# Optimization experiments

Hardware: AMD Instinct MI355X
Metric: run time of the kernel (lower is better)

## Reference

```python
import jax, jax.numpy as jnp
import numpy as np

N_NODES = 100000


def gcn_conv(x, W, b, src, dst, num_nodes):
    # PyG GCNConv: add self-loops, symmetric deg^-1/2 normalization,
    # linear transform, scatter-add aggregation at dst, then bias.
    loop = jnp.arange(num_nodes, dtype=src.dtype)
    row = jnp.concatenate([src, loop])  # message sources
    col = jnp.concatenate([dst, loop])  # message destinations
    deg = jax.ops.segment_sum(jnp.ones_like(col, dtype=x.dtype), col,
                              num_segments=num_nodes)
    dinv = jnp.where(deg > 0, jax.lax.rsqrt(deg), 0.0)
    norm = dinv[row] * dinv[col]  # [E+N]
    h = x @ W  # [N, out]
    msg = h[row] * norm[:, None]  # gather + scale, [E+N, out]
    out = jax.ops.segment_sum(msg, col, num_segments=num_nodes)  # scatter-add
    return out + b


def setup_inputs() -> dict:
    key = jax.random.key(0)
    k1, k2, k3, k4, k5, k6 = jax.random.split(key, 6)
    dim_in, dim_h = 256, 128
    E = 1600000
    x = jax.random.normal(k1, (N_NODES, dim_in), dtype=jnp.float32)
    edge_index = jax.random.randint(k2, (2, E), 0, N_NODES, dtype=jnp.int64)
    # Glorot-style init for GCNConv weights
    W1 = jax.random.normal(k3, (dim_in, dim_h), dtype=jnp.float32) * (1.0 / np.sqrt(dim_in))
    b1 = jnp.zeros((dim_h,), dtype=jnp.float32)
    W2 = jax.random.normal(k4, (dim_h, 1), dtype=jnp.float32) * (1.0 / np.sqrt(dim_h))
    b2 = jnp.zeros((1,), dtype=jnp.float32)
    return {"x": x, "edge_index": edge_index, "W1": W1, "b1": b1, "W2": W2, "b2": b2}


def reference(x, edge_index, W1, b1, W2, b2):
    src, dst = edge_index[0], edge_index[1]
    h = gcn_conv(x, W1, b1, src, dst, N_NODES)
    h = jax.nn.relu(h)
    h = gcn_conv(h, W2, b2, src, dst, N_NODES)
    return jax.nn.sigmoid(h)  # [N, 1]
```

## Files before the change

kernel.cpp:

```cpp
#include <hip/hip_runtime.h>
#include <math.h>

#define NN 100000
#define DIN 256
#define DH 128
#define GEMM_NB 1563
#define BSHIFT 9
#define BNODES 512
#define NB_BUCKET 196
#define BCAP 12288
#define PA_EDGES 8192
#define PREP_NB 64

using short8  = __attribute__((ext_vector_type(8))) short;
using float4v = __attribute__((ext_vector_type(4))) float;

static __device__ __forceinline__ unsigned short f2bf(float f) {
    unsigned u = __float_as_uint(f);
    unsigned r = u + 0x7fffu + ((u >> 16) & 1u);
    return (unsigned short)(r >> 16);
}
static __device__ __forceinline__ float bf_lo(unsigned u) { return __uint_as_float(u << 16); }
static __device__ __forceinline__ float bf_hi(unsigned u) { return __uint_as_float(u & 0xffff0000u); }

__global__ __launch_bounds__(512) void k_prep_partA(const float* __restrict__ W1,
                                                    unsigned short* __restrict__ W1p,
                                                    const int* __restrict__ src,
                                                    const int* __restrict__ dst, int E,
                                                    int* __restrict__ bucketFill,
                                                    int2* __restrict__ bucketArr) {
    __shared__ int aCnt[NB_BUCKET];
    __shared__ int aBase[NB_BUCKET];
    const int tid = threadIdx.x;

    if (blockIdx.x < PREP_NB) {
        int t = blockIdx.x * 512 + tid;
        int lane = t & 63;
        int ks   = (t >> 6) & 7;
        int nt   = (t >> 9) & 1;
        int wv   = (t >> 10) & 3;
        int n = wv * 32 + nt * 16 + (lane & 15);
        int kbase = ks * 32 + (lane >> 4) * 8;
        short8 v;
#pragma unroll
        for (int j = 0; j < 8; ++j) v[j] = (short)f2bf(W1[(kbase + j) * DH + n]);
        *(short8*)&W1p[(long long)t * 8] = v;
        return;
    }

    const int ba = blockIdx.x - PREP_NB;
    for (int i = tid; i < NB_BUCKET; i += 512) aCnt[i] = 0;
    __syncthreads();
    const int e0   = ba * PA_EDGES;
    const int eend = min(e0 + PA_EDGES, E);
    for (int e = e0 + tid; e < eend; e += 512)
        atomicAdd(&aCnt[dst[e] >> BSHIFT], 1);
    __syncthreads();
    for (int i = tid; i < NB_BUCKET; i += 512) {
        int c = aCnt[i];
        aBase[i] = c ? atomicAdd(&bucketFill[i], c) : 0;
        aCnt[i] = 0;
    }
    __syncthreads();
    for (int e = e0 + tid; e < eend; e += 512) {
        int d = dst[e];
        int b = d >> BSHIFT;
        int r = atomicAdd(&aCnt[b], 1);
        bucketArr[(long long)b * BCAP + aBase[b] + r] = make_int2(src[e], d);
    }
}

__global__ __launch_bounds__(512) void k_gemm_partB(const float* __restrict__ x,
                                                    const unsigned short* __restrict__ W1p,
                                                    unsigned short* __restrict__ hs,
                                                    const int* __restrict__ bucketFill,
                                                    const int2* __restrict__ bucketArr,
                                                    int* __restrict__ cnt,
                                                    int* __restrict__ excl,
                                                    float* __restrict__ dinv,
                                                    int* __restrict__ eidx) {
    __shared__ unsigned short aL[64 * 32 * 8];
    __shared__ int h[BNODES];
    __shared__ int hex[BNODES];
    __shared__ int st[256];
    const int tid = threadIdx.x;

    if (blockIdx.x < NB_BUCKET) {
        const int b     = blockIdx.x;
        const int nbase = b << BSHIFT;
        const int len   = bucketFill[b];
        const long long abase = (long long)b * BCAP;

        if (tid < 256) st[tid] = (tid < b) ? bucketFill[tid] : 0;
        __syncthreads();
        for (int off = 128; off > 0; off >>= 1) {
            if (tid < off) st[tid] += st[tid + off];
            __syncthreads();
        }
        const int gbase = st[0];
        __syncthreads();

        for (int i = tid; i < BNODES; i += 512) h[i] = 0;
        __syncthreads();
        for (int k = tid; k < len; k += 512)
            atomicAdd(&h[bucketArr[abase + k].y - nbase], 1);
        __syncthreads();

        int a0 = 0, a1 = 0;
        if (tid < 256) {
            a0 = h[2 * tid]; a1 = h[2 * tid + 1];
            st[tid] = a0 + a1;
        }
        __syncthreads();
        for (int off = 1; off < 256; off <<= 1) {
            int val = (tid < 256 && tid >= off) ? st[tid - off] : 0;
            __syncthreads();
            if (tid < 256) st[tid] += val;
            __syncthreads();
        }
        if (tid < 256) {
            int prev = (tid > 0) ? st[tid - 1] : 0;
            hex[2 * tid]     = prev;
            hex[2 * tid + 1] = prev + a0;
        }
        __syncthreads();

        for (int i = tid; i < BNODES; i += 512) {
            int n = nbase + i;
            if (n < NN) {
                int c = h[i];
                cnt[n]  = c;
                excl[n] = gbase + hex[i];
                dinv[n] = rsqrtf(1.0f + (float)c);
            }
        }
        for (int i = tid; i < BNODES; i += 512) h[i] = 0;
        __syncthreads();

        for (int k = tid; k < len; k += 512) {
            int2 p = bucketArr[abase + k];
            int li = p.y - nbase;
            int r = atomicAdd(&h[li], 1);
            eidx[gbase + hex[li] + r] = p.x;
        }
        return;
    }

    const int bid  = blockIdx.x - NB_BUCKET;
    const int w8   = tid >> 6;
    const int lane = tid & 63;
    const int quad = lane >> 4;
    const int m16  = lane & 15;
    const int row0 = bid * 64;

    short8 bfr[8];
#pragma unroll
    for (int ks = 0; ks < 8; ++ks)
        bfr[ks] = ((const short8*)W1p)[(w8 * 8 + ks) * 64 + lane];

#pragma unroll
    for (int it = 0; it < 4; ++it) {
        int id  = it * 512 + tid;
        int row = id >> 5;
        int kb  = id & 31;
        int gr  = row0 + row;
        float4 f0, f1;
        if (gr < NN) {
            const float* xp = &x[(long long)gr * DIN + kb * 8];
            f0 = *(const float4*)xp;
            f1 = *(const float4*)(xp + 4);
        } else {
            f0 = make_float4(0.f, 0.f, 0.f, 0.f);
            f1 = f0;
        }
        short8 v;
        v[0] = (short)f2bf(f0.x); v[1] = (short)f2bf(f0.y);
        v[2] = (short)f2bf(f0.z); v[3] = (short)f2bf(f0.w);
        v[4] = (short)f2bf(f1.x); v[5] = (short)f2bf(f1.y);
        v[6] = (short)f2bf(f1.z); v[7] = (short)f2bf(f1.w);
        int chunk = row * 32 + (kb ^ (row & 31));
        *(short8*)&aL[chunk * 8] = v;
    }
    __syncthreads();

    float4v acc[4];
#pragma unroll
    for (int mt = 0; mt < 4; ++mt) acc[mt] = (float4v)(0.0f);

#pragma unroll
    for (int mt = 0; mt < 4; ++mt) {
        int row = mt * 16 + m16;
#pragma unroll
        for (int ks = 0; ks < 8; ++ks) {
            int kb = ks * 4 + quad;
            int chunk = row * 32 + (kb ^ (row & 31));
            short8 a = *(const short8*)&aL[chunk * 8];
            acc[mt] = __builtin_amdgcn_mfma_f32_16x16x32_bf16(a, bfr[ks], acc[mt], 0, 0, 0);
        }
    }

    const int n0 = w8 * 16;
#pragma unroll
    for (int mt = 0; mt < 4; ++mt) {
#pragma unroll
        for (int r = 0; r < 4; ++r) {
            int row = row0 + mt * 16 + quad * 4 + r;
            if (row < NN)
                hs[(long long)row * DH + n0 + m16] = f2bf(acc[mt][r]);
        }
    }
}

__global__ __launch_bounds__(256) void k_agg1l2(const int* __restrict__ eidx,
                                                const int* __restrict__ excl,
                                                const int* __restrict__ cnt,
                                                const unsigned* __restrict__ hs2,
                                                const float* __restrict__ dinv,
                                                const float* __restrict__ b1,
                                                const float* __restrict__ W2,
                                                float* __restrict__ zs) {
    int w = (blockIdx.x * 256 + threadIdx.x) >> 6;
    if (w >= NN) return;
    int lane = threadIdx.x & 63;
    int offs = __builtin_amdgcn_readfirstlane(excl[w]);
    int c    = __builtin_amdgcn_readfirstlane(cnt[w]);

    float dw = dinv[w];
    unsigned u = hs2[(long long)w * 64 + lane];
    float ax = dw * bf_lo(u);
    float ay = dw * bf_hi(u);

    const int l16 = lane & 15;
    for (int j = 0; j < c; j += 16) {
        int rem = c - j; if (rem > 16) rem = 16;
        int idx = offs + j + ((l16 < rem) ? l16 : 0);
        int sv = eidx[idx];
        float es[16]; unsigned uu[16];
#pragma unroll
        for (int q = 0; q < 16; ++q) if (q < rem) {
            int sq = __builtin_amdgcn_readlane(sv, q);
            es[q] = dinv[sq];
            uu[q] = hs2[(long long)sq * 64 + lane];
        }
#pragma unroll
        for (int q = 0; q < 16; ++q) if (q < rem) {
            ax = fmaf(es[q], bf_lo(uu[q]), ax);
            ay = fmaf(es[q], bf_hi(uu[q]), ay);
        }
    }

    float2 bb = ((const float2*)b1)[lane];
    float2 ww = ((const float2*)W2)[lane];
    float r0 = fmaxf(fmaf(dw, ax, bb.x), 0.0f);
    float r1 = fmaxf(fmaf(dw, ay, bb.y), 0.0f);
    float v = r0 * ww.x + r1 * ww.y;
#pragma unroll
    for (int off = 32; off > 0; off >>= 1) v += __shfl_down(v, off);
    if (lane == 0) zs[w] = v * dw;
}

__global__ void k_agg2_final(const int* __restrict__ eidx,
                             const int* __restrict__ excl,
                             const int* __restrict__ cnt,
                             const float* __restrict__ zs,
                             const float* __restrict__ dinv,
                             const float* __restrict__ b2,
                             float* __restrict__ out) {
    int i = blockIdx.x * 256 + threadIdx.x;
    if (i >= NN) return;
    int offs = excl[i];
    int c = cnt[i];
    float v = zs[i];
    int j = 0;
    for (; j + 3 < c; j += 4) {
        int s0 = eidx[offs + j + 0];
        int s1 = eidx[offs + j + 1];
        int s2 = eidx[offs + j + 2];
        int s3 = eidx[offs + j + 3];
        v += zs[s0] + zs[s1] + zs[s2] + zs[s3];
    }
    for (; j < c; ++j) v += zs[eidx[offs + j]];
    float z = fmaf(dinv[i], v, b2[0]);
    out[i] = 1.0f / (1.0f + __expf(-z));
}

extern "C" void kernel_launch(void* const* d_in, const int* in_sizes, int n_in,
                              void* d_out, int out_size, void* d_ws, size_t ws_size,
                              hipStream_t stream) {
    const float* x  = (const float*)d_in[0];
    const int*   ei = (const int*)d_in[1];
    const float* W1 = (const float*)d_in[2];
    const float* b1 = (const float*)d_in[3];
    const float* W2 = (const float*)d_in[4];
    const float* b2 = (const float*)d_in[5];
    float* out = (float*)d_out;

    const int E = in_sizes[1] / 2;
    const int* src = ei;
    const int* dst = ei + E;

    int* wsi = (int*)d_ws;
    float* dinv       = (float*)wsi;
    int*   cnt        = wsi + NN;
    int*   excl       = cnt + NN;
    float* zs         = (float*)(excl + NN);
    int*   bucketFill = (int*)(zs + NN);
    unsigned short* W1p = (unsigned short*)(bucketFill + 256);
    int*   eidx       = (int*)(W1p + 32768);
    int2*  bucketArr  = (int2*)(eidx + E);
    unsigned short* hs = (unsigned short*)(bucketArr + (long long)NB_BUCKET * BCAP);

    const int nb_nodes = (NN + 255) / 256;
    const int pa_nb = (E + PA_EDGES - 1) / PA_EDGES;

    hipMemsetAsync(bucketFill, 0, NB_BUCKET * sizeof(int), stream);

    k_prep_partA<<<PREP_NB + pa_nb, 512, 0, stream>>>(W1, W1p, src, dst, E,
                                                      bucketFill, bucketArr);
    k_gemm_partB<<<NB_BUCKET + GEMM_NB, 512, 0, stream>>>(x, W1p, hs, bucketFill, bucketArr,
                                                          cnt, excl, dinv, eidx);

    k_agg1l2<<<(NN * 64 + 255) / 256, 256, 0, stream>>>(eidx, excl, cnt,
                                                        (const unsigned*)hs, dinv, b1, W2, zs);

    k_agg2_final<<<nb_nodes, 256, 0, stream>>>(eidx, excl, cnt, zs, dinv, b2, out);
}
```

Baseline: 325.8 us.

## Split wavefront into two half-waves each gathering alternate neighbor rows with 8-byte loads

The layer-1 aggregation kernel now has each 64-lane wavefront work as two 32-lane halves. Each half handles alternate edges and loads 4 bf16 features per lane as uint2. The halves' partial sums are combined with a cross-half shuffle before the bias, ReLU and W2 dot product. This aims to double the number of independent row gathers in flight and to widen each load, cutting latency-bound gather time. It drops the readlane/scalar broadcast of edge indices, so each lane now loads indices and dinv itself, which adds per-lane memory traffic and a reduction step.

```diff
diff --git a/kernel.cpp b/kernel.cpp
--- a/kernel.cpp
+++ b/kernel.cpp
@@ -221,41 +221,72 @@
                                                 float* __restrict__ zs) {
     int w = (blockIdx.x * 256 + threadIdx.x) >> 6;
     if (w >= NN) return;
-    int lane = threadIdx.x & 63;
-    int offs = __builtin_amdgcn_readfirstlane(excl[w]);
-    int c    = __builtin_amdgcn_readfirstlane(cnt[w]);
+    const int lane = threadIdx.x & 63;
+    const int hh   = lane >> 5;
+    const int l5   = lane & 31;
+    int offs = excl[w];
+    int c    = cnt[w];
 
     float dw = dinv[w];
-    unsigned u = hs2[(long long)w * 64 + lane];
-    float ax = dw * bf_lo(u);
-    float ay = dw * bf_hi(u);
-
-    const int l16 = lane & 15;
-    for (int j = 0; j < c; j += 16) {
-        int rem = c - j; if (rem > 16) rem = 16;
-        int idx = offs + j + ((l16 < rem) ? l16 : 0);
-        int sv = eidx[idx];
-        float es[16]; unsigned uu[16];
-#pragma unroll
-        for (int q = 0; q < 16; ++q) if (q < rem) {
-            int sq = __builtin_amdgcn_readlane(sv, q);
-            es[q] = dinv[sq];
-            uu[q] = hs2[(long long)sq * 64 + lane];
-        }
-#pragma unroll
-        for (int q = 0; q < 16; ++q) if (q < rem) {
-            ax = fmaf(es[q], bf_lo(uu[q]), ax);
-            ay = fmaf(es[q], bf_hi(uu[q]), ay);
-        }
-    }
-
-    float2 bb = ((const float2*)b1)[lane];
-    float2 ww = ((const float2*)W2)[lane];
-    float r0 = fmaxf(fmaf(dw, ax, bb.x), 0.0f);
-    float r1 = fmaxf(fmaf(dw, ay, bb.y), 0.0f);
-    float v = r0 * ww.x + r1 * ww.y;
-#pragma unroll
-    for (int off = 32; off > 0; off >>= 1) v += __shfl_down(v, off);
+    const uint2* hrow = (const uint2*)hs2;
+
+    uint2 su = hrow[(long long)w * 32 + l5];
+    float ss = hh ? 0.0f : dw;
+    float a0 = ss * bf_lo(su.x);
+    float a1 = ss * bf_hi(su.x);
+    float a2 = ss * bf_lo(su.y);
+    float a3 = ss * bf_hi(su.y);
+
+    int j = 0;
+    for (; j + 7 < c; j += 8) {
+        int s[4]; float es[4]; uint2 uu[4];
+#pragma unroll
+        for (int q = 0; q < 4; ++q) s[q] = eidx[offs + j + 2 * q + hh];
+#pragma unroll
+        for (int q = 0; q < 4; ++q) es[q] = dinv[s[q]];
+#pragma unroll
+        for (int q = 0; q < 4; ++q) uu[q] = hrow[(long long)s[q] * 32 + l5];
+#pragma unroll
+        for (int q = 0; q < 4; ++q) {
+            a0 = fmaf(es[q], bf_lo(uu[q].x), a0);
+            a1 = fmaf(es[q], bf_hi(uu[q].x), a1);
+            a2 = fmaf(es[q], bf_lo(uu[q].y), a2);
+            a3 = fmaf(es[q], bf_hi(uu[q].y), a3);
+        }
+    }
+    for (; j + 1 < c; j += 2) {
+        int s0 = eidx[offs + j + hh];
+        float e0 = dinv[s0];
+        uint2 u0 = hrow[(long long)s0 * 32 + l5];
+        a0 = fmaf(e0, bf_lo(u0.x), a0);
+        a1 = fmaf(e0, bf_hi(u0.x), a1);
+        a2 = fmaf(e0, bf_lo(u0.y), a2);
+        a3 = fmaf(e0, bf_hi(u0.y), a3);
+    }
+    if (j < c) {
+        int s0 = eidx[offs + j];
+        float e0 = hh ? 0.0f : dinv[s0];
+        uint2 u0 = hrow[(long long)s0 * 32 + l5];
+        a0 = fmaf(e0, bf_lo(u0.x), a0);
+        a1 = fmaf(e0, bf_hi(u0.x), a1);
+        a2 = fmaf(e0, bf_lo(u0.y), a2);
+        a3 = fmaf(e0, bf_hi(u0.y), a3);
+    }
+
+    a0 += __shfl_xor(a0, 32);
+    a1 += __shfl_xor(a1, 32);
+    a2 += __shfl_xor(a2, 32);
+    a3 += __shfl_xor(a3, 32);
+
+    float4 bb = ((const float4*)b1)[l5];
+    float4 ww = ((const float4*)W2)[l5];
+    float r0 = fmaxf(fmaf(dw, a0, bb.x), 0.0f);
+    float r1 = fmaxf(fmaf(dw, a1, bb.y), 0.0f);
+    float r2 = fmaxf(fmaf(dw, a2, bb.z), 0.0f);
+    float r3 = fmaxf(fmaf(dw, a3, bb.w), 0.0f);
+    float v = r0 * ww.x + r1 * ww.y + r2 * ww.z + r3 * ww.w;
+#pragma unroll
+    for (int off = 16; off > 0; off >>= 1) v += __shfl_down(v, off);
     if (lane == 0) zs[w] = v * dw;
 }
 
```

Measured after the change: 288.2 us. 11.5% less time.

## Slice hidden features into 16-column planes and split layer-1 aggregation across slices

Applied to the files above, without the earlier changes.

The GEMM now writes its bf16 hidden output as eight column slices, each a contiguous [N,16] plane, so each slice fits in a smaller region of cache. The layer-1 aggregation runs one block group per slice, with 16 edges handled in parallel per wave (4 lanes per 8-byte feature chunk), then a shuffle reduction. Partial layer-2 dot products are combined with atomicAdd into a zero-initialised zs buffer, which the enlarged memset covers. Nontemporal loads are added for streaming reads of x, src and eidx. The trade-off is extra atomics and re-reading the edge lists eight times in exchange for better cache locality of the gathered features.

```diff
diff --git a/kernel.cpp b/kernel.cpp
--- a/kernel.cpp
+++ b/kernel.cpp
@@ -65,8 +65,9 @@
     for (int e = e0 + tid; e < eend; e += 512) {
         int d = dst[e];
         int b = d >> BSHIFT;
+        int s = __builtin_nontemporal_load(&src[e]);
         int r = atomicAdd(&aCnt[b], 1);
-        bucketArr[(long long)b * BCAP + aBase[b] + r] = make_int2(src[e], d);
+        bucketArr[(long long)b * BCAP + aBase[b] + r] = make_int2(s, d);
     }
 }
 
@@ -164,20 +165,20 @@
         int row = id >> 5;
         int kb  = id & 31;
         int gr  = row0 + row;
-        float4 f0, f1;
+        float4v f0, f1;
         if (gr < NN) {
-            const float* xp = &x[(long long)gr * DIN + kb * 8];
-            f0 = *(const float4*)xp;
-            f1 = *(const float4*)(xp + 4);
+            const float4v* xp = (const float4v*)&x[(long long)gr * DIN + kb * 8];
+            f0 = __builtin_nontemporal_load(xp);
+            f1 = __builtin_nontemporal_load(xp + 1);
         } else {
-            f0 = make_float4(0.f, 0.f, 0.f, 0.f);
-            f1 = f0;
+            f0 = (float4v)(0.0f);
+            f1 = (float4v)(0.0f);
         }
         short8 v;
-        v[0] = (short)f2bf(f0.x); v[1] = (short)f2bf(f0.y);
-        v[2] = (short)f2bf(f0.z); v[3] = (short)f2bf(f0.w);
-        v[4] = (short)f2bf(f1.x); v[5] = (short)f2bf(f1.y);
-        v[6] = (short)f2bf(f1.z); v[7] = (short)f2bf(f1.w);
+        v[0] = (short)f2bf(f0[0]); v[1] = (short)f2bf(f0[1]);
+        v[2] = (short)f2bf(f0[2]); v[3] = (short)f2bf(f0[3]);
+        v[4] = (short)f2bf(f1[0]); v[5] = (short)f2bf(f1[1]);
+        v[6] = (short)f2bf(f1[2]); v[7] = (short)f2bf(f1[3]);
         int chunk = row * 32 + (kb ^ (row & 31));
         *(short8*)&aL[chunk * 8] = v;
     }
@@ -199,14 +200,13 @@
         }
     }
 
-    const int n0 = w8 * 16;
 #pragma unroll
     for (int mt = 0; mt < 4; ++mt) {
 #pragma unroll
         for (int r = 0; r < 4; ++r) {
             int row = row0 + mt * 16 + quad * 4 + r;
             if (row < NN)
-                hs[(long long)row * DH + n0 + m16] = f2bf(acc[mt][r]);
+                hs[((long long)w8 * NN + row) * 16 + m16] = f2bf(acc[mt][r]);
         }
     }
 }
@@ -214,49 +214,61 @@
 __global__ __launch_bounds__(256) void k_agg1l2(const int* __restrict__ eidx,
                                                 const int* __restrict__ excl,
                                                 const int* __restrict__ cnt,
-                                                const unsigned* __restrict__ hs2,
+                                                const unsigned* __restrict__ hs_s,
                                                 const float* __restrict__ dinv,
                                                 const float* __restrict__ b1,
                                                 const float* __restrict__ W2,
                                                 float* __restrict__ zs) {
-    int w = (blockIdx.x * 256 + threadIdx.x) >> 6;
-    if (w >= NN) return;
-    int lane = threadIdx.x & 63;
-    int offs = __builtin_amdgcn_readfirstlane(excl[w]);
-    int c    = __builtin_amdgcn_readfirstlane(cnt[w]);
-
-    float dw = dinv[w];
-    unsigned u = hs2[(long long)w * 64 + lane];
-    float ax = dw * bf_lo(u);
-    float ay = dw * bf_hi(u);
-
-    const int l16 = lane & 15;
-    for (int j = 0; j < c; j += 16) {
-        int rem = c - j; if (rem > 16) rem = 16;
-        int idx = offs + j + ((l16 < rem) ? l16 : 0);
-        int sv = eidx[idx];
-        float es[16]; unsigned uu[16];
-#pragma unroll
-        for (int q = 0; q < 16; ++q) if (q < rem) {
-            int sq = __builtin_amdgcn_readlane(sv, q);
-            es[q] = dinv[sq];
-            uu[q] = hs2[(long long)sq * 64 + lane];
-        }
-#pragma unroll
-        for (int q = 0; q < 16; ++q) if (q < rem) {
-            ax = fmaf(es[q], bf_lo(uu[q]), ax);
-            ay = fmaf(es[q], bf_hi(uu[q]), ay);
-        }
-    }
-
-    float2 bb = ((const float2*)b1)[lane];
-    float2 ww = ((const float2*)W2)[lane];
-    float r0 = fmaxf(fmaf(dw, ax, bb.x), 0.0f);
-    float r1 = fmaxf(fmaf(dw, ay, bb.y), 0.0f);
-    float v = r0 * ww.x + r1 * ww.y;
-#pragma unroll
-    for (int off = 32; off > 0; off >>= 1) v += __shfl_down(v, off);
-    if (lane == 0) zs[w] = v * dw;
+    const int bid   = blockIdx.x;
+    const int slice = bid & 7;
+    const int g     = bid >> 3;
+    const int tid   = threadIdx.x;
+    const int lane  = tid & 63;
+    const int wv    = tid >> 6;
+    const int f4    = lane & 3;
+    const int e16   = lane >> 2;
+    const uint2* hrow = (const uint2*)hs_s + (long long)slice * NN * 4;
+
+    const float4 bb = ((const float4*)b1)[slice * 4 + f4];
+    const float4 ww = ((const float4*)W2)[slice * 4 + f4];
+
+    const int wbase = (g * 4 + wv) * 8;
+    for (int ni = 0; ni < 8; ++ni) {
+        int w = wbase + ni;
+        if (w >= NN) break;
+        int offs = excl[w];
+        int c    = cnt[w];
+        float dw = dinv[w];
+        float a0 = 0.f, a1 = 0.f, a2 = 0.f, a3 = 0.f;
+        for (int j = 0; j <= c; j += 16) {
+            int  eq    = j + e16;
+            bool valid = (eq <= c);
+            int  ld    = offs + ((valid && eq > 0) ? (eq - 1) : 0);
+            int  sR    = __builtin_nontemporal_load(&eidx[ld]);
+            int  s     = (valid && eq > 0) ? sR : w;
+            float e    = valid ? dinv[s] : 0.0f;
+            uint2 u    = hrow[(long long)s * 4 + f4];
+            a0 = fmaf(e, bf_lo(u.x), a0);
+            a1 = fmaf(e, bf_hi(u.x), a1);
+            a2 = fmaf(e, bf_lo(u.y), a2);
+            a3 = fmaf(e, bf_hi(u.y), a3);
+        }
+#pragma unroll
+        for (int m = 4; m <= 32; m <<= 1) {
+            a0 += __shfl_xor(a0, m);
+            a1 += __shfl_xor(a1, m);
+            a2 += __shfl_xor(a2, m);
+            a3 += __shfl_xor(a3, m);
+        }
+        float r0 = fmaxf(fmaf(dw, a0, bb.x), 0.0f);
+        float r1 = fmaxf(fmaf(dw, a1, bb.y), 0.0f);
+        float r2 = fmaxf(fmaf(dw, a2, bb.z), 0.0f);
+        float r3 = fmaxf(fmaf(dw, a3, bb.w), 0.0f);
+        float v = r0 * ww.x + r1 * ww.y + r2 * ww.z + r3 * ww.w;
+        v += __shfl_xor(v, 1);
+        v += __shfl_xor(v, 2);
+        if (lane == 0) atomicAdd(&zs[w], dw * v);
+    }
 }
 
 __global__ void k_agg2_final(const int* __restrict__ eidx,
@@ -273,10 +285,10 @@
     float v = zs[i];
     int j = 0;
     for (; j + 3 < c; j += 4) {
-        int s0 = eidx[offs + j + 0];
-        int s1 = eidx[offs + j + 1];
-        int s2 = eidx[offs + j + 2];
-        int s3 = eidx[offs + j + 3];
+        int s0 = __builtin_nontemporal_load(&eidx[offs + j + 0]);
+        int s1 = __builtin_nontemporal_load(&eidx[offs + j + 1]);
+        int s2 = __builtin_nontemporal_load(&eidx[offs + j + 2]);
+        int s3 = __builtin_nontemporal_load(&eidx[offs + j + 3]);
         v += zs[s0] + zs[s1] + zs[s2] + zs[s3];
     }
     for (; j < c; ++j) v += zs[eidx[offs + j]];
@@ -313,15 +325,15 @@
     const int nb_nodes = (NN + 255) / 256;
     const int pa_nb = (E + PA_EDGES - 1) / PA_EDGES;
 
-    hipMemsetAsync(bucketFill, 0, NB_BUCKET * sizeof(int), stream);
+    hipMemsetAsync(zs, 0, (NN + NB_BUCKET) * sizeof(int), stream);
 
     k_prep_partA<<<PREP_NB + pa_nb, 512, 0, stream>>>(W1, W1p, src, dst, E,
                                                       bucketFill, bucketArr);
     k_gemm_partB<<<NB_BUCKET + GEMM_NB, 512, 0, stream>>>(x, W1p, hs, bucketFill, bucketArr,
                                                           cnt, excl, dinv, eidx);
 
-    k_agg1l2<<<(NN * 64 + 255) / 256, 256, 0, stream>>>(eidx, excl, cnt,
-                                                        (const unsigned*)hs, dinv, b1, W2, zs);
+    k_agg1l2<<<8 * ((NN + 31) / 32), 256, 0, stream>>>(eidx, excl, cnt,
+                                                       (const unsigned*)hs, dinv, b1, W2, zs);
 
     k_agg2_final<<<nb_nodes, 256, 0, stream>>>(eidx, excl, cnt, zs, dinv, b2, out);
 }
```

Result: slower. 497.9 us (+52.8%).
